# Kernel optimization log

Measured on AMD Instinct MI355X. Metric: run time of the kernel, lower is better.

Reference implementation:

```python
import jax, jax.numpy as jnp
import numpy as np


def setup_inputs() -> dict:
    key = jax.random.key(0)
    k1, k2 = jax.random.split(key)
    B, C, H, W = 32, 256, 32, 32
    K = 2048
    x = jax.random.normal(k1, (B, C, H, W), dtype=jnp.float32)
    # nn.Embedding init in source is uniform(-1/K, 1/K); use normal scaled similarly-small
    embed_w = jax.random.uniform(k2, (K, C), dtype=jnp.float32, minval=-1.0 / K, maxval=1.0 / K)
    return {"x": x, "embed_w": embed_w}


def reference(x, embed_w):
    # x: [B, C, H, W] -> tokens [B, HW, C]
    B, C, H, W = x.shape
    tokens = jnp.transpose(x, (0, 2, 3, 1)).reshape(B, H * W, C)
    # Euclidean argmin: argmin_k ||t - e_k||^2 = argmin_k (||e_k||^2 - 2 t.e_k)
    # Avoids materializing sqrt cdist; argmin is identical.
    e_sq = jnp.sum(embed_w * embed_w, axis=-1)           # [K]
    dots = jnp.einsum('bnc,kc->bnk', tokens, embed_w)    # [B, HW, K] dominant intermediate
    embed_idx = jnp.argmin(e_sq[None, None, :] - 2.0 * dots, axis=-1)  # [B, HW]
    # one-hot matmul in source == gather
    quantized = embed_w[embed_idx]                        # [B, HW, C]
    quantize = jnp.transpose(quantized.reshape(B, H, W, C), (0, 3, 1, 2))  # [B, C, H, W]
    embed_index = embed_idx.reshape(B, H, W)
    loss = jnp.zeros((1,), dtype=jnp.float32)  # eval path: loss stays 0
    return quantize, embed_index, loss
```

## Files before the change

kernel.cpp:

```cpp
#include <hip/hip_runtime.h>


#define CDIM 256
#define KDIM 2048
#define HW   1024
#define NTOK 32768
#define QOFF 8388608
#define LOFF (QOFF + NTOK)

typedef _Float16 f16x8 __attribute__((ext_vector_type(8)));
typedef float    f32x4 __attribute__((ext_vector_type(4)));

__device__ __forceinline__ f16x8 ld16(const char* p) { return *(const f16x8*)(p); }

__global__ __launch_bounds__(256) void prep_kernel(const float* __restrict__ x,
                                                   const float* __restrict__ ew,
                                                   char* __restrict__ Aws,
                                                   char* __restrict__ Ews,
                                                   float* __restrict__ esq,
                                                   float* __restrict__ out) {
    __shared__ float tile[32][257];
    const int t = threadIdx.x;
    if (blockIdx.x < 1024) {
        const int bid = blockIdx.x;
        const int b = bid >> 5;
        const int kc = (bid >> 2) & 7;
        const int c0 = kc * 32;
        const int hw0 = (bid & 3) * 256;
        #pragma unroll 8
        for (int r = 0; r < 32; ++r)
            tile[r][t] = x[((size_t)(b * CDIM + c0 + r) << 10) + hw0 + t];
        __syncthreads();
        union { _Float16 h[32]; uint4 q[4]; } Hb, Lb;
        #pragma unroll 8
        for (int r = 0; r < 32; ++r) {
            const float xs = tile[r][t] * 64.0f;
            const _Float16 hh = (_Float16)xs;
            Hb.h[r] = hh;
            Lb.h[r] = (_Float16)(xs - (float)hh);
        }
        const int tok = b * HW + hw0 + t;
        const int p = tok >> 6, row = tok & 63;
        char* d = Aws + (size_t)p * 65536 + kc * 8192 + row * 16;
        #pragma unroll
        for (int g = 0; g < 4; ++g) {
            *(uint4*)(d + g * 1024)        = Hb.q[g];
            *(uint4*)(d + 4096 + g * 1024) = Lb.q[g];
        }
    } else {
        const int bid = blockIdx.x - 1024;
        const int code = bid * 8 + (t >> 5);
        const int u = t & 31;
        const float4 v0 = *(const float4*)&ew[(size_t)code * CDIM + u * 8];
        const float4 v1 = *(const float4*)&ew[(size_t)code * CDIM + u * 8 + 4];
        float s = v0.x*v0.x + v0.y*v0.y + v0.z*v0.z + v0.w*v0.w
                + v1.x*v1.x + v1.y*v1.y + v1.z*v1.z + v1.w*v1.w;
        #pragma unroll
        for (int m = 16; m >= 1; m >>= 1) s += __shfl_xor(s, m, 32);
        if (u == 0) esq[code] = s * 2097152.0f;
        const float e[8] = {v0.x, v0.y, v0.z, v0.w, v1.x, v1.y, v1.z, v1.w};
        union { _Float16 h[8]; uint4 q; } H, L;
        #pragma unroll
        for (int j = 0; j < 8; ++j) {
            const float ev = e[j] * 32768.0f;
            const _Float16 hh = (_Float16)ev;
            H.h[j] = hh;
            L.h[j] = (_Float16)(ev - (float)hh);
        }
        const int kc = u >> 2, g = u & 3;
        const int p = code >> 6, row = code & 63;
        char* d = Ews + (size_t)p * 65536 + kc * 8192 + g * 1024 + row * 16;
        *(uint4*)d = H.q;
        *(uint4*)(d + 4096) = L.q;
        if (bid == 0 && t == 0) out[LOFF] = 0.0f;
    }
}

__global__ __launch_bounds__(256, 3) void vqmm_kernel(const char* __restrict__ Aws,
                                                      const char* __restrict__ Ews,
                                                      const float* __restrict__ esq,
                                                      float* __restrict__ cv,
                                                      int* __restrict__ ci) {
    __shared__ __align__(16) char elds[32768];

    const int t = threadIdx.x;
    const int bid = blockIdx.x;
    const int by = (bid & 7) | ((bid >> 8) << 3);
    const int bx = (bid >> 3) & 31;
    const int lane = t & 63, w = t >> 6;
    const int g = lane >> 4, lr = lane & 15;
    const int kc0 = (bid + w) & 3;

    const char* pa = Aws + (size_t)(by * 4 + w) * 65536 + g * 1024 + lr * 16;
    const char* esrc = Ews + (size_t)bx * 65536;

    f16x8 fa[4], fb[4], ec[4], ed[4];
    {
        const char* pa0 = pa + kc0 * 8192;
        #pragma unroll
        for (int m = 0; m < 4; ++m) {
            fa[m] = ld16(pa0 + m * 256);
            fb[m] = ld16(pa0 + 4096 + m * 256);
        }
    }
    #pragma unroll
    for (int j = 0; j < 8; ++j) {
        const int off = j * 4096 + t * 16;
        *(uint4*)(elds + off) = *(const uint4*)(esrc + off);
    }
    __syncthreads();

    const f32x4 zf = {0.f, 0.f, 0.f, 0.f};
    f32x4 acc[4][4];
    #pragma unroll
    for (int m = 0; m < 4; ++m)
        #pragma unroll
        for (int n = 0; n < 4; ++n) acc[m][n] = zf;

    const char* el0 = elds + g * 1024 + lr * 16;
    {
        const char* ep0 = el0 + kc0 * 8192;
        #pragma unroll
        for (int n = 0; n < 4; ++n) {
            ec[n] = ld16(ep0 + n * 256);
            ed[n] = ld16(ep0 + 4096 + n * 256);
        }
    }

    #pragma unroll
    for (int h = 0; h < 2; ++h) {
        if (h == 1) {
            __syncthreads();
            #pragma unroll
            for (int j = 0; j < 8; ++j) {
                const int off = j * 4096 + t * 16;
                *(uint4*)(elds + off) = *(const uint4*)(esrc + 32768 + off);
            }
            __syncthreads();
            const char* ep = el0 + kc0 * 8192;
            #pragma unroll
            for (int n = 0; n < 4; ++n) {
                ec[n] = ld16(ep + n * 256);
                ed[n] = ld16(ep + 4096 + n * 256);
            }
        }
        #pragma unroll
        for (int i = 0; i < 4; ++i) {
            const bool lastA = (h == 1) && (i == 3);
            const int gkcn = (i < 3) ? (h * 4 + ((kc0 + i + 1) & 3)) : (4 + kc0);
            const char* pan = pa + gkcn * 8192;
            #pragma unroll
            for (int m = 0; m < 4; ++m) {
                __builtin_amdgcn_s_setprio(1);
                #pragma unroll
                for (int n = 0; n < 4; ++n) {
                    acc[m][n] = __builtin_amdgcn_mfma_f32_16x16x32_f16(fa[m], ec[n], acc[m][n], 0, 0, 0);
                    acc[m][n] = __builtin_amdgcn_mfma_f32_16x16x32_f16(fa[m], ed[n], acc[m][n], 0, 0, 0);
                    acc[m][n] = __builtin_amdgcn_mfma_f32_16x16x32_f16(fb[m], ec[n], acc[m][n], 0, 0, 0);
                }
                __builtin_amdgcn_s_setprio(0);
                if (!lastA) {
                    fa[m] = ld16(pan + m * 256);
                    fb[m] = ld16(pan + 4096 + m * 256);
                }
            }
            if (i < 3) {
                const char* en = el0 + ((kc0 + i + 1) & 3) * 8192;
                #pragma unroll
                for (int n = 0; n < 4; ++n) {
                    ec[n] = ld16(en + n * 256);
                    ed[n] = ld16(en + 4096 + n * 256);
                }
            }
        }
    }

    float eq[4];
    #pragma unroll
    for (int n = 0; n < 4; ++n) eq[n] = esq[bx * 64 + n * 16 + lr];
    #pragma unroll
    for (int m = 0; m < 4; ++m) {
        #pragma unroll
        for (int r = 0; r < 4; ++r) {
            float bv = 3.4e38f; int bi = 0x7fffffff;
            #pragma unroll
            for (int n = 0; n < 4; ++n) {
                const float d = fmaf(-2.0f, acc[m][n][r], eq[n]);
                const int cidx = bx * 64 + n * 16 + lr;
                if (d < bv) { bv = d; bi = cidx; }
            }
            #pragma unroll
            for (int mk = 1; mk < 16; mk <<= 1) {
                const float ov = __shfl_xor(bv, mk, 16);
                const int   oi = __shfl_xor(bi, mk, 16);
                if (ov < bv || (ov == bv && oi < bi)) { bv = ov; bi = oi; }
            }
            if (lr == 0) {
                const size_t o = (size_t)bx * NTOK + by * 256 + w * 64 + m * 16 + g * 4 + r;
                cv[o] = bv; ci[o] = bi;
            }
        }
    }
}

__global__ __launch_bounds__(256) void merge_gather_kernel(const float* __restrict__ cv,
                                                           const int* __restrict__ ci,
                                                           const float* __restrict__ ew,
                                                           float* __restrict__ out) {
    __shared__ int sIdx[64];
    const int t = threadIdx.x;
    const int n0 = blockIdx.x * 64;
    if (t < 64) {
        const int tok = n0 + t;
        float bv = cv[tok]; int bi = ci[tok];
        #pragma unroll
        for (int s = 1; s < 32; ++s) {
            const float v = cv[(size_t)s * NTOK + tok];
            const int   i2 = ci[(size_t)s * NTOK + tok];
            if (v < bv || (v == bv && i2 < bi)) { bv = v; bi = i2; }
        }
        sIdx[t] = bi;
        out[QOFF + tok] = (float)bi;
    }
    __syncthreads();
    const int b = n0 >> 10, hw0 = n0 & (HW - 1);
    const int i = t & 63, cg = t >> 6;
    const int kidx = sIdx[i];
    const float* er = ew + (size_t)kidx * CDIM;
    float* ob = out + (size_t)b * CDIM * HW + hw0 + i;
    #pragma unroll
    for (int p = 0; p < CDIM / 4; ++p) {
        const int c = cg * 64 + p;
        ob[(size_t)c * HW] = er[c];
    }
}

extern "C" void kernel_launch(void* const* d_in, const int* in_sizes, int n_in,
                              void* d_out, int out_size, void* d_ws, size_t ws_size,
                              hipStream_t stream) {
    const float* x  = (const float*)d_in[0];
    const float* ew = (const float*)d_in[1];
    float* out = (float*)d_out;
    char* ws = (char*)d_ws;

    char*  Aws = ws;
    char*  Ews = ws + 33554432;
    float* esq = (float*)(ws + 35651584);
    float* cvv = (float*)(ws + 35659776);
    int*   cii = (int*)(ws + 39854080);

    prep_kernel<<<1280, 256, 0, stream>>>(x, ew, Aws, Ews, esq, out);
    vqmm_kernel<<<4096, 256, 0, stream>>>(Aws, Ews, esq, cvv, cii);
    merge_gather_kernel<<<NTOK / 64, 256, 0, stream>>>(cvv, cii, ew, out);
}
```

Before: 145.9 us.

## Double-buffer embedding tiles in LDS and parallelize partial-argmin merge

The GEMM kernel now streams the 64KB embedding tile in four 16KB quarters. Each next quarter is prefetched into registers while MFMAs run on the current LDS buffer, replacing the two blocking half-tile reloads bracketed by barriers. The merge kernel spreads the 32-way partial argmin reduction across all 256 threads and finishes through shared memory, instead of 64 threads each doing 32 serial loads. This adds register pressure from the uint4 staging buffers and an extra barrier per quarter.

```diff
diff --git a/kernel.cpp b/kernel.cpp
--- a/kernel.cpp
+++ b/kernel.cpp
@@ -89,14 +89,19 @@
     const int bx = (bid >> 3) & 31;
     const int lane = t & 63, w = t >> 6;
     const int g = lane >> 4, lr = lane & 15;
-    const int kc0 = (bid + w) & 3;
+    const int r = (bid + w) & 1;
 
     const char* pa = Aws + (size_t)(by * 4 + w) * 65536 + g * 1024 + lr * 16;
     const char* esrc = Ews + (size_t)bx * 65536;
 
     f16x8 fa[4], fb[4], ec[4], ed[4];
+    uint4 rg[4];
+
+    #pragma unroll
+    for (int j = 0; j < 4; ++j)
+        rg[j] = *(const uint4*)(esrc + j * 4096 + t * 16);
     {
-        const char* pa0 = pa + kc0 * 8192;
+        const char* pa0 = pa + r * 8192;
         #pragma unroll
         for (int m = 0; m < 4; ++m) {
             fa[m] = ld16(pa0 + m * 256);
@@ -104,10 +109,8 @@
         }
     }
     #pragma unroll
-    for (int j = 0; j < 8; ++j) {
-        const int off = j * 4096 + t * 16;
-        *(uint4*)(elds + off) = *(const uint4*)(esrc + off);
-    }
+    for (int j = 0; j < 4; ++j)
+        *(uint4*)(elds + j * 4096 + t * 16) = rg[j];
     __syncthreads();
 
     const f32x4 zf = {0.f, 0.f, 0.f, 0.f};
@@ -117,9 +120,8 @@
         #pragma unroll
         for (int n = 0; n < 4; ++n) acc[m][n] = zf;
 
-    const char* el0 = elds + g * 1024 + lr * 16;
     {
-        const char* ep0 = el0 + kc0 * 8192;
+        const char* ep0 = elds + r * 8192 + g * 1024 + lr * 16;
         #pragma unroll
         for (int n = 0; n < 4; ++n) {
             ec[n] = ld16(ep0 + n * 256);
@@ -128,16 +130,16 @@
     }
 
     #pragma unroll
-    for (int h = 0; h < 2; ++h) {
-        if (h == 1) {
-            __syncthreads();
-            #pragma unroll
-            for (int j = 0; j < 8; ++j) {
-                const int off = j * 4096 + t * 16;
-                *(uint4*)(elds + off) = *(const uint4*)(esrc + 32768 + off);
-            }
-            __syncthreads();
-            const char* ep = el0 + kc0 * 8192;
+    for (int q = 0; q < 4; ++q) {
+        const int buf = (q & 1) * 16384;
+        if (q < 3) {
+            const char* s2 = esrc + (q + 1) * 16384;
+            #pragma unroll
+            for (int j = 0; j < 4; ++j)
+                rg[j] = *(const uint4*)(s2 + j * 4096 + t * 16);
+        }
+        if (q > 0) {
+            const char* ep = elds + buf + r * 8192 + g * 1024 + lr * 16;
             #pragma unroll
             for (int n = 0; n < 4; ++n) {
                 ec[n] = ld16(ep + n * 256);
@@ -145,10 +147,10 @@
             }
         }
         #pragma unroll
-        for (int i = 0; i < 4; ++i) {
-            const bool lastA = (h == 1) && (i == 3);
-            const int gkcn = (i < 3) ? (h * 4 + ((kc0 + i + 1) & 3)) : (4 + kc0);
-            const char* pan = pa + gkcn * 8192;
+        for (int p = 0; p < 2; ++p) {
+            const bool lastPhase = (q == 3) && (p == 1);
+            const int kcA = (p == 0) ? (2 * q + (r ^ 1)) : (2 * (q + 1) + r);
+            const char* pan = pa + kcA * 8192;
             #pragma unroll
             for (int m = 0; m < 4; ++m) {
                 __builtin_amdgcn_s_setprio(1);
@@ -159,13 +161,13 @@
                     acc[m][n] = __builtin_amdgcn_mfma_f32_16x16x32_f16(fb[m], ec[n], acc[m][n], 0, 0, 0);
                 }
                 __builtin_amdgcn_s_setprio(0);
-                if (!lastA) {
+                if (!lastPhase) {
                     fa[m] = ld16(pan + m * 256);
                     fb[m] = ld16(pan + 4096 + m * 256);
                 }
             }
-            if (i < 3) {
-                const char* en = el0 + ((kc0 + i + 1) & 3) * 8192;
+            if (p == 0) {
+                const char* en = elds + buf + (r ^ 1) * 8192 + g * 1024 + lr * 16;
                 #pragma unroll
                 for (int n = 0; n < 4; ++n) {
                     ec[n] = ld16(en + n * 256);
@@ -173,6 +175,13 @@
                 }
             }
         }
+        if (q < 3) {
+            char* nb = elds + ((q + 1) & 1) * 16384;
+            #pragma unroll
+            for (int j = 0; j < 4; ++j)
+                *(uint4*)(nb + j * 4096 + t * 16) = rg[j];
+            __syncthreads();
+        }
     }
 
     float eq[4];
@@ -181,11 +190,11 @@
     #pragma unroll
     for (int m = 0; m < 4; ++m) {
         #pragma unroll
-        for (int r = 0; r < 4; ++r) {
+        for (int rr = 0; rr < 4; ++rr) {
             float bv = 3.4e38f; int bi = 0x7fffffff;
             #pragma unroll
             for (int n = 0; n < 4; ++n) {
-                const float d = fmaf(-2.0f, acc[m][n][r], eq[n]);
+                const float d = fmaf(-2.0f, acc[m][n][rr], eq[n]);
                 const int cidx = bx * 64 + n * 16 + lr;
                 if (d < bv) { bv = d; bi = cidx; }
             }
@@ -196,7 +205,7 @@
                 if (ov < bv || (ov == bv && oi < bi)) { bv = ov; bi = oi; }
             }
             if (lr == 0) {
-                const size_t o = (size_t)bx * NTOK + by * 256 + w * 64 + m * 16 + g * 4 + r;
+                const size_t o = (size_t)bx * NTOK + by * 256 + w * 64 + m * 16 + g * 4 + rr;
                 cv[o] = bv; ci[o] = bi;
             }
         }
@@ -207,20 +216,33 @@
                                                            const int* __restrict__ ci,
                                                            const float* __restrict__ ew,
                                                            float* __restrict__ out) {
-    __shared__ int sIdx[64];
+    __shared__ float redV[256];
+    __shared__ int   redI[256];
+    __shared__ int   sIdx[64];
     const int t = threadIdx.x;
     const int n0 = blockIdx.x * 64;
+    {
+        const int tok = n0 + (t & 63);
+        const int s0 = (t >> 6) * 8;
+        float bv = 3.4e38f; int bi = 0x7fffffff;
+        #pragma unroll
+        for (int s = 0; s < 8; ++s) {
+            const float v  = cv[(size_t)(s0 + s) * NTOK + tok];
+            const int   i2 = ci[(size_t)(s0 + s) * NTOK + tok];
+            if (v < bv || (v == bv && i2 < bi)) { bv = v; bi = i2; }
+        }
+        redV[t] = bv; redI[t] = bi;
+    }
+    __syncthreads();
     if (t < 64) {
-        const int tok = n0 + t;
-        float bv = cv[tok]; int bi = ci[tok];
-        #pragma unroll
-        for (int s = 1; s < 32; ++s) {
-            const float v = cv[(size_t)s * NTOK + tok];
-            const int   i2 = ci[(size_t)s * NTOK + tok];
+        float bv = redV[t]; int bi = redI[t];
+        #pragma unroll
+        for (int s = 1; s < 4; ++s) {
+            const float v = redV[t + s * 64]; const int i2 = redI[t + s * 64];
             if (v < bv || (v == bv && i2 < bi)) { bv = v; bi = i2; }
         }
         sIdx[t] = bi;
-        out[QOFF + tok] = (float)bi;
+        out[QOFF + n0 + t] = (float)bi;
     }
     __syncthreads();
     const int b = n0 >> 10, hw0 = n0 & (HW - 1);
```

New measurement: 135.2 us (median of 3 runs). 1.08x faster.
